# Kernel optimization log

Measured on AMD Instinct MI355X. Metric: run time of the kernel, lower is better.

## Reference

```python
import jax, jax.numpy as jnp
import numpy as np
from jax import lax

B, SEQ, CIN = 8, 4096, 7
DM, NL, PL = 512, 4, 16
NP = SEQ // PL            # 256 patches
NS, DC, EXP = 16, 4, 2
DI = EXP * DM             # 1024 inner dim
DTR = (DM + 15) // 16     # 32 dt_rank (mamba_ssm default ceil(d_model/16))
CD, PRED = 64, 96
EPS = 1e-5


def setup_inputs() -> dict:
    key = jax.random.key(0)
    ks = jax.random.split(key, 16)
    r = lambda k, s, sc=0.02: jax.random.normal(k, s, jnp.float32) * sc
    A_row = jnp.arange(1, NS + 1, dtype=jnp.float32)
    return {
        "x": jax.random.normal(ks[0], (B, SEQ, CIN), jnp.float32),
        "in_g": jnp.ones((CIN,), jnp.float32), "in_b": jnp.zeros((CIN,), jnp.float32),
        "pe_W": r(ks[1], (DM, CIN, PL), 0.1), "pe_b": jnp.zeros((DM,), jnp.float32),
        "ln_g": jnp.ones((NL, DM), jnp.float32), "ln_b": jnp.zeros((NL, DM), jnp.float32),
        "W_in": r(ks[2], (NL, 2 * DI, DM)),
        "conv_W": r(ks[3], (NL, DI, 1, DC), 0.2), "conv_b": jnp.zeros((NL, DI), jnp.float32),
        "W_x": r(ks[4], (NL, DTR + 2 * NS, DI)),
        "W_dt": r(ks[5], (NL, DI, DTR), 0.1),
        "b_dt": jnp.full((NL, DI), -4.6, jnp.float32),  # softplus^-1(~0.01)
        "A_log": jnp.log(jnp.tile(A_row, (NL, DI, 1))),
        "Dskip": jnp.ones((NL, DI), jnp.float32),
        "W_out": r(ks[6], (NL, DM, DI)),
        "fn_g": jnp.ones((DM,), jnp.float32), "fn_b": jnp.zeros((DM,), jnp.float32),
        "hW1": r(ks[7], (2 * CD, DM * NP)), "hb1": jnp.zeros((2 * CD,), jnp.float32),
        "hW2": r(ks[8], (PRED, 2 * CD)), "hb2": jnp.zeros((PRED,), jnp.float32),
    }


def layernorm(x, g, b):
    m = jnp.mean(x, axis=-1, keepdims=True)
    v = jnp.mean((x - m) ** 2, axis=-1, keepdims=True)
    return (x - m) * lax.rsqrt(v + EPS) * g + b


def silu(x):
    return x * jax.nn.sigmoid(x)


def selective_scan(dA, dBx, C):
    # dA, dBx: (B, L, DI, N);  C: (B, L, N)  ->  y: (B, L, DI)
    def step(h, t):
        dA_t, dbx_t, c_t = t
        h = dA_t * h + dbx_t                      # (B, DI, N)
        y = jnp.einsum('bdn,bn->bd', h, c_t)
        return h, y
    h0 = jnp.zeros((dA.shape[0], DI, NS), dA.dtype)
    _, ys = lax.scan(step, h0, (dA.transpose(1, 0, 2, 3), dBx.transpose(1, 0, 2, 3), C.transpose(1, 0, 2)))
    return ys.transpose(1, 0, 2)


def mamba_block(u, W_in, cW, cb, W_x, W_dt, b_dt, A_log, Dv, W_out):
    xz = jnp.einsum('bld,ed->ble', u, W_in)       # (B, L, 2*DI)
    xi, z = jnp.split(xz, 2, axis=-1)
    # causal depthwise conv over time
    xc = lax.conv_general_dilated(xi.transpose(0, 2, 1), cW, (1,), [(DC - 1, 0)],
                                  feature_group_count=DI,
                                  dimension_numbers=('NCH', 'OIH', 'NCH'))
    xc = silu(xc + cb[None, :, None]).transpose(0, 2, 1)  # (B, L, DI)
    dbl = jnp.einsum('bld,ed->ble', xc, W_x)      # (B, L, DTR + 2*NS)
    dt, Bm, Cm = dbl[..., :DTR], dbl[..., DTR:DTR + NS], dbl[..., DTR + NS:]
    delta = jax.nn.softplus(jnp.einsum('blr,dr->bld', dt, W_dt) + b_dt)  # (B, L, DI)
    A = -jnp.exp(A_log)                           # (DI, NS)
    dA = jnp.exp(delta[..., None] * A)            # (B, L, DI, NS)
    dBx = delta[..., None] * Bm[:, :, None, :] * xc[..., None]
    y = selective_scan(dA, dBx, Cm)
    y = (y + xc * Dv) * silu(z)
    return jnp.einsum('bld,od->blo', y, W_out)


def reference(x, in_g, in_b, pe_W, pe_b, ln_g, ln_b, W_in, conv_W, conv_b,
              W_x, W_dt, b_dt, A_log, Dskip, W_out, fn_g, fn_b, hW1, hb1, hW2, hb2):
    h = layernorm(x, in_g, in_b)
    # patch embed: stride==kernel Conv1d == per-patch matmul
    p = h.reshape(B, NP, PL, CIN)
    h = jnp.einsum('bnpc,dcp->bnd', p, pe_W) + pe_b   # (B, NP, DM)
    for i in range(NL):
        res = h
        h = layernorm(h, ln_g[i], ln_b[i])
        h = mamba_block(h, W_in[i], conv_W[i], conv_b[i], W_x[i], W_dt[i],
                        b_dt[i], A_log[i], Dskip[i], W_out[i])
        h = h + res                                   # dropout is identity at eval
    h = layernorm(h, fn_g, fn_b)
    h = h.reshape(B, -1)                              # (B, DM*NP)
    h = jax.nn.gelu(h @ hW1.T + hb1, approximate=False)
    return h @ hW2.T + hb2                            # (B, PRED)
```

## Files before the change

kernel.cpp:

```cpp
#include <hip/hip_runtime.h>
#include <hip/hip_bf16.h>
#include <math.h>

#define B_    8
#define SEQ_  4096
#define CIN_  7
#define DM_   512
#define NL_   4
#define PL_   16
#define NP_   256
#define NS_   16
#define DC_   4
#define DI_   1024
#define DTR_  32
#define CD_   64
#define PRED_ 96
#define TOK_  (B_*NP_)
#define EPS_  1e-5f
#define CL_   16
#define NCH_  (NP_/CL_)

typedef unsigned short u16;
typedef __attribute__((ext_vector_type(8))) short short8;
typedef __attribute__((ext_vector_type(4))) float floatx4;

__device__ __forceinline__ float silu_f(float x){ return x / (1.f + __expf(-x)); }
__device__ __forceinline__ float softplus_f(float x){ return x > 20.f ? x : log1pf(__expf(x)); }
__device__ __forceinline__ u16 f2bf(float f){
  union { __hip_bfloat16 h; u16 u; } cv; cv.h = __float2bfloat16(f); return cv.u;
}
#define GLDS16(g, l) __builtin_amdgcn_global_load_lds( \
    (const __attribute__((address_space(1))) void*)(g), \
    (__attribute__((address_space(3))) void*)(l), 16, 0, 0)

__global__ void ln7_kernel(const float* __restrict__ x, const float* __restrict__ g,
                           const float* __restrict__ b, u16* __restrict__ xpb){
  int i = blockIdx.x*256 + threadIdx.x;
  if (i >= B_*SEQ_) return;
  float v[CIN_]; float m = 0.f;
  #pragma unroll
  for (int c=0;c<CIN_;c++){ v[c]=x[i*CIN_+c]; m+=v[c]; }
  m *= (1.f/CIN_);
  float var = 0.f;
  #pragma unroll
  for (int c=0;c<CIN_;c++){ float d=v[c]-m; var+=d*d; }
  var *= (1.f/CIN_);
  float r = rsqrtf(var + EPS_);
  int bn = i >> 4, p = i & 15;
  u16* row = xpb + (size_t)bn*128;
  #pragma unroll
  for (int c=0;c<CIN_;c++) row[c*16+p] = f2bf((v[c]-m)*r*g[c]+b[c]);
  row[112+p] = 0;
}

__global__ __launch_bounds__(256) void ln512_kernel(const float* __restrict__ in,
    const float* __restrict__ g, const float* __restrict__ b,
    float* __restrict__ out, u16* __restrict__ outb){
  int tid = threadIdx.x;
  int wv = tid>>6, lane = tid&63;
  int t = blockIdx.x*4 + wv;
  const float4* row = (const float4*)(in + (size_t)t*DM_);
  float4 v0 = row[lane], v1 = row[64+lane];
  float s = v0.x+v0.y+v0.z+v0.w + v1.x+v1.y+v1.z+v1.w;
  #pragma unroll
  for (int o=1;o<64;o<<=1) s += __shfl_xor(s,o);
  float m = s*(1.f/DM_);
  float d0x=v0.x-m,d0y=v0.y-m,d0z=v0.z-m,d0w=v0.w-m;
  float d1x=v1.x-m,d1y=v1.y-m,d1z=v1.z-m,d1w=v1.w-m;
  float q = d0x*d0x+d0y*d0y+d0z*d0z+d0w*d0w + d1x*d1x+d1y*d1y+d1z*d1z+d1w*d1w;
  #pragma unroll
  for (int o=1;o<64;o<<=1) q += __shfl_xor(q,o);
  float r = rsqrtf(q*(1.f/DM_) + EPS_);
  float4 g0 = ((const float4*)g)[lane], g1 = ((const float4*)g)[64+lane];
  float4 b0 = ((const float4*)b)[lane], b1 = ((const float4*)b)[64+lane];
  float4 o0 = { d0x*r*g0.x+b0.x, d0y*r*g0.y+b0.y, d0z*r*g0.z+b0.z, d0w*r*g0.w+b0.w };
  float4 o1 = { d1x*r*g1.x+b1.x, d1y*r*g1.y+b1.y, d1z*r*g1.z+b1.z, d1w*r*g1.w+b1.w };
  ((float4*)(out + (size_t)t*DM_))[lane]    = o0;
  ((float4*)(out + (size_t)t*DM_))[64+lane] = o1;
  ushort4 p0 = { f2bf(o0.x), f2bf(o0.y), f2bf(o0.z), f2bf(o0.w) };
  ushort4 p1 = { f2bf(o1.x), f2bf(o1.y), f2bf(o1.z), f2bf(o1.w) };
  ((ushort4*)(outb + (size_t)t*DM_))[lane]    = p0;
  ((ushort4*)(outb + (size_t)t*DM_))[64+lane] = p1;
}

template<int BM, int BN, bool ACC, bool BIAS>
__global__ __launch_bounds__(256) void gemm_bf16(const u16* __restrict__ A,
    const u16* __restrict__ Bw, float* __restrict__ C, const float* __restrict__ bias,
    int K, int lda, int ldb, int ldc){
  constexpr int MI = BM/32, NI = BN/32;
  __shared__ __align__(16) u16 As[BM*64];
  __shared__ __align__(16) u16 Bs[BN*64];
  int tid = threadIdx.x;
  int wave = __builtin_amdgcn_readfirstlane(tid>>6);
  int lane = tid&63;
  int wm = wave>>1, wn = wave&1;
  int quad = lane>>4, l16 = lane&15;
  int bm = blockIdx.y*BM, bn = blockIdx.x*BN;
  int r8 = lane>>3, sseg = lane&7;
  int gseg = sseg ^ r8;
  floatx4 acc[MI][NI] = {};
  for (int k0 = 0; k0 < K; k0 += 64){
    #pragma unroll
    for (int r = 0; r < BM/32; r++){
      int rowb = (r*4 + wave)*8;
      const u16* gp = A + (size_t)(bm + rowb + r8)*lda + k0 + gseg*8;
      GLDS16(gp, &As[rowb*64]);
    }
    #pragma unroll
    for (int r = 0; r < BN/32; r++){
      int rowb = (r*4 + wave)*8;
      const u16* gp = Bw + (size_t)(bn + rowb + r8)*ldb + k0 + gseg*8;
      GLDS16(gp, &Bs[rowb*64]);
    }
    __syncthreads();
    #pragma unroll
    for (int kh = 0; kh < 2; kh++){
      short8 af[MI], bfr[NI];
      #pragma unroll
      for (int i = 0; i < MI; i++){
        int row = wm*(BM/2)+i*16+l16;
        af[i] = *(short8*)&As[row*64 + (((kh*4+quad)^(row&7))*8)];
      }
      #pragma unroll
      for (int j = 0; j < NI; j++){
        int row = wn*(BN/2)+j*16+l16;
        bfr[j] = *(short8*)&Bs[row*64 + (((kh*4+quad)^(row&7))*8)];
      }
      #pragma unroll
      for (int i = 0; i < MI; i++)
        #pragma unroll
        for (int j = 0; j < NI; j++)
          acc[i][j] = __builtin_amdgcn_mfma_f32_16x16x32_bf16(af[i], bfr[j], acc[i][j], 0, 0, 0);
    }
    __syncthreads();
  }
  #pragma unroll
  for (int i = 0; i < MI; i++){
    #pragma unroll
    for (int j = 0; j < NI; j++){
      #pragma unroll
      for (int r = 0; r < 4; r++){
        int m  = bm + wm*(BM/2) + i*16 + quad*4 + r;
        int nn = bn + wn*(BN/2) + j*16 + l16;
        float v = acc[i][j][r];
        if (ACC) C[(size_t)m*ldc+nn] += v;
        else     C[(size_t)m*ldc+nn]  = BIAS ? v + bias[nn] : v;
      }
    }
  }
}

__global__ __launch_bounds__(256) void mid_kernel(
    const float* __restrict__ xz, const float* __restrict__ cW, const float* __restrict__ cb,
    const float* __restrict__ wxT, const float* __restrict__ wdtT, const float* __restrict__ bdt,
    float* __restrict__ xc, float* __restrict__ dblo, float* __restrict__ delta){
  __shared__ float sxc[8*1024];
  __shared__ float swx[64*68];
  __shared__ float sdbl[8][64];
  int tid = threadIdx.x;
  int t0 = blockIdx.x*8;
  int l0 = t0 & (NP_-1);
  int c = tid*4;
  float w0[4], w1[4], w2[4], w3[4];
  *(float4*)w0 = *(const float4*)&cW[(c+0)*DC_];
  *(float4*)w1 = *(const float4*)&cW[(c+1)*DC_];
  *(float4*)w2 = *(const float4*)&cW[(c+2)*DC_];
  *(float4*)w3 = *(const float4*)&cW[(c+3)*DC_];
  float4 bias4 = *(const float4*)&cb[c];
  #pragma unroll
  for (int r = 0; r < 8; r++){
    float4 acc = bias4;
    int l = l0 + r;
    #pragma unroll
    for (int k = 0; k < DC_; k++){
      if (l - 3 + k >= 0){
        float4 xv = *(const float4*)&xz[(size_t)(t0 + r + k - 3)*(2*DI_) + c];
        acc.x += xv.x*w0[k]; acc.y += xv.y*w1[k]; acc.z += xv.z*w2[k]; acc.w += xv.w*w3[k];
      }
    }
    acc.x = silu_f(acc.x); acc.y = silu_f(acc.y); acc.z = silu_f(acc.z); acc.w = silu_f(acc.w);
    *(float4*)&sxc[r*1024 + c] = acc;
    *(float4*)&xc[(size_t)(t0+r)*DI_ + c] = acc;
  }
  int lane = tid & 63, wv = tid >> 6;
  int ta = wv*2, tb = ta + 1;
  float acc0 = 0.f, acc1 = 0.f;
  __syncthreads();
  for (int k0 = 0; k0 < DI_; k0 += 64){
    #pragma unroll
    for (int i = tid; i < 1024; i += 256){
      int k = i >> 4, e4 = (i & 15)*4;
      float4 v = *(const float4*)&wxT[(size_t)(k0 + k)*64 + e4];
      swx[(e4+0)*68 + k] = v.x;
      swx[(e4+1)*68 + k] = v.y;
      swx[(e4+2)*68 + k] = v.z;
      swx[(e4+3)*68 + k] = v.w;
    }
    __syncthreads();
    #pragma unroll
    for (int k4 = 0; k4 < 64; k4 += 4){
      float4 wq = *(float4*)&swx[lane*68 + k4];
      float4 xa = *(float4*)&sxc[ta*1024 + k0 + k4];
      float4 xb = *(float4*)&sxc[tb*1024 + k0 + k4];
      acc0 += xa.x*wq.x + xa.y*wq.y + xa.z*wq.z + xa.w*wq.w;
      acc1 += xb.x*wq.x + xb.y*wq.y + xb.z*wq.z + xb.w*wq.w;
    }
    __syncthreads();
  }
  sdbl[ta][lane] = acc0;
  sdbl[tb][lane] = acc1;
  dblo[(size_t)(t0+ta)*64 + lane] = acc0;
  dblo[(size_t)(t0+tb)*64 + lane] = acc1;
  __syncthreads();
  #pragma unroll
  for (int dc = 0; dc < 4; dc++){
    int d = dc*256 + tid;
    float wr[DTR_];
    #pragma unroll
    for (int r = 0; r < DTR_; r++) wr[r] = wdtT[(size_t)r*DI_ + d];
    float bb = bdt[d];
    #pragma unroll
    for (int t = 0; t < 8; t++){
      float acc = bb;
      #pragma unroll
      for (int r = 0; r < DTR_; r++) acc += sdbl[t][r]*wr[r];
      delta[(size_t)(t0+t)*DI_ + d] = softplus_f(acc);
    }
  }
}

__global__ __launch_bounds__(256) void scan_part_kernel(const float* __restrict__ delta,
    const float* __restrict__ xc, const float* __restrict__ dbl,
    const float* __restrict__ Alog, float* __restrict__ hend, float* __restrict__ aprod){
  __shared__ float sBC[CL_][32];
  int tid = threadIdx.x;
  int d = blockIdx.x*256 + tid;
  int bych = blockIdx.y;
  int b = bych >> 4, ch = bych & (NCH_-1);
  int base = b*NP_ + ch*CL_;
  for (int i = tid; i < CL_*32; i += 256){
    int t = i >> 5, c = i & 31;
    sBC[t][c] = dbl[(size_t)(base+t)*64 + 32 + c];
  }
  float A[NS_], h[NS_], pr[NS_];
  #pragma unroll
  for (int k = 0; k < NS_; k++){
    A[k] = -__expf(Alog[(size_t)d*NS_ + k]);
    h[k] = 0.f; pr[k] = 1.f;
  }
  __syncthreads();
  #pragma unroll
  for (int t = 0; t < CL_; t++){
    int row = base + t;
    float de = delta[(size_t)row*DI_ + d];
    float xv = xc[(size_t)row*DI_ + d];
    float cde = de*xv;
    #pragma unroll
    for (int k = 0; k < NS_; k++){
      float a = __expf(de*A[k]);
      h[k] = a*h[k] + cde*sBC[t][k];
      pr[k] *= a;
    }
  }
  size_t o = ((size_t)bych*DI_ + d)*NS_;
  #pragma unroll
  for (int k = 0; k < NS_; k++){ hend[o+k] = h[k]; aprod[o+k] = pr[k]; }
}

__global__ __launch_bounds__(256) void scan_fix_kernel(const float* __restrict__ aprod,
    float* __restrict__ hend){
  int id = blockIdx.x*256 + threadIdx.x;
  int nd = id & (DI_*NS_ - 1);
  int b  = id >> 14;
  float h = 0.f;
  #pragma unroll
  for (int ch = 0; ch < NCH_; ch++){
    size_t idx = (size_t)(b*NCH_ + ch)*(DI_*NS_) + nd;
    float ap = aprod[idx];
    float he = hend[idx];
    hend[idx] = h;
    h = ap*h + he;
  }
}

__global__ __launch_bounds__(256) void scan_final_kernel(const float* __restrict__ delta,
    const float* __restrict__ xc, const float* __restrict__ dbl,
    const float* __restrict__ xz, const float* __restrict__ Dv,
    const float* __restrict__ Alog, const float* __restrict__ hin,
    u16* __restrict__ yb){
  __shared__ float sBC[CL_][32];
  int tid = threadIdx.x;
  int d = blockIdx.x*256 + tid;
  int bych = blockIdx.y;
  int b = bych >> 4, ch = bych & (NCH_-1);
  int base = b*NP_ + ch*CL_;
  for (int i = tid; i < CL_*32; i += 256){
    int t = i >> 5, c = i & 31;
    sBC[t][c] = dbl[(size_t)(base+t)*64 + 32 + c];
  }
  float A[NS_], h[NS_];
  size_t o = ((size_t)bych*DI_ + d)*NS_;
  #pragma unroll
  for (int k = 0; k < NS_; k++){
    A[k] = -__expf(Alog[(size_t)d*NS_ + k]);
    h[k] = hin[o + k];
  }
  float Dvd = Dv[d];
  __syncthreads();
  #pragma unroll
  for (int t = 0; t < CL_; t++){
    int row = base + t;
    float de = delta[(size_t)row*DI_ + d];
    float xv = xc[(size_t)row*DI_ + d];
    float zz = xz[(size_t)row*(2*DI_) + DI_ + d];
    float cde = de*xv;
    float p = 0.f;
    #pragma unroll
    for (int k = 0; k < NS_; k++){
      float a = __expf(de*A[k]);
      h[k] = a*h[k] + cde*sBC[t][k];
      p += h[k]*sBC[t][16+k];
    }
    yb[(size_t)row*DI_ + d] = f2bf((p + xv*Dvd) * silu_f(zz));
  }
}

__global__ __launch_bounds__(256) void head1_kernel(const float* __restrict__ u,
    const float* __restrict__ hW1, float* __restrict__ partial){
  const int KTOT = DM_*NP_;
  int nb = blockIdx.x;
  int kc = blockIdx.y;
  int tid = threadIdx.x;
  int lane = tid & 63, wv = tid >> 6;
  int k = kc*1024 + tid*4;
  float4 uv[8];
  #pragma unroll
  for (int m = 0; m < 8; m++) uv[m] = *(const float4*)&u[(size_t)m*KTOT + k];
  float acc[8][8];
  #pragma unroll
  for (int n = 0; n < 8; n++){
    float4 wv4 = *(const float4*)&hW1[(size_t)(nb*8+n)*KTOT + k];
    #pragma unroll
    for (int m = 0; m < 8; m++)
      acc[n][m] = uv[m].x*wv4.x + uv[m].y*wv4.y + uv[m].z*wv4.z + uv[m].w*wv4.w;
  }
  __shared__ float red[4][64];
  #pragma unroll
  for (int n = 0; n < 8; n++){
    #pragma unroll
    for (int m = 0; m < 8; m++){
      float v = acc[n][m];
      v += __shfl_xor(v,1); v += __shfl_xor(v,2); v += __shfl_xor(v,4);
      v += __shfl_xor(v,8); v += __shfl_xor(v,16); v += __shfl_xor(v,32);
      if (lane == 0) red[wv][n*8+m] = v;
    }
  }
  __syncthreads();
  if (tid < 64){
    float s = red[0][tid] + red[1][tid] + red[2][tid] + red[3][tid];
    int n = tid >> 3, m = tid & 7;
    partial[((size_t)kc*128 + nb*8 + n)*8 + m] = s;
  }
}

__global__ void head_combine_kernel(const float* __restrict__ partial,
    const float* __restrict__ hb1, float* __restrict__ t1){
  int idx = blockIdx.x*256 + threadIdx.x;
  if (idx >= 128*8) return;
  int n = idx >> 3, m = idx & 7;
  float s = hb1[n];
  for (int kc = 0; kc < 128; kc++) s += partial[((size_t)kc*128 + n)*8 + m];
  float ge = 0.5f*s*(1.f + erff(s*0.70710678118f));
  t1[m*128 + n] = ge;
}

__global__ void head2_kernel(const float* __restrict__ t1, const float* __restrict__ hW2,
                             const float* __restrict__ hb2, float* __restrict__ out){
  int idx = blockIdx.x*128 + threadIdx.x;
  if (idx >= B_*PRED_) return;
  int m = idx / PRED_, q = idx % PRED_;
  float s = hb2[q];
  #pragma unroll 16
  for (int k = 0; k < 2*CD_; k++) s += t1[m*128 + k]*hW2[q*128 + k];
  out[idx] = s;
}

__global__ __launch_bounds__(256) void prep_kernel(const float* __restrict__ W_dt,
    const float* __restrict__ W_x, const float* __restrict__ W_in,
    const float* __restrict__ W_out, const float* __restrict__ peW,
    float* __restrict__ wdtT, float* __restrict__ wxT,
    u16* __restrict__ WinB, u16* __restrict__ WoutB, u16* __restrict__ peWb){
  int idx = blockIdx.x*256 + threadIdx.x;
  {
    float4 v = ((const float4*)W_in)[idx];
    ushort4 o = { f2bf(v.x), f2bf(v.y), f2bf(v.z), f2bf(v.w) };
    ((ushort4*)WinB)[idx] = o;
  }
  if (idx < 524288){
    float4 v = ((const float4*)W_out)[idx];
    ushort4 o = { f2bf(v.x), f2bf(v.y), f2bf(v.z), f2bf(v.w) };
    ((ushort4*)WoutB)[idx] = o;
  }
  if (idx < NL_*DTR_*DI_){
    int l = idx / (DTR_*DI_); int rem = idx % (DTR_*DI_);
    int r = rem / DI_; int d = rem % DI_;
    wdtT[idx] = W_dt[((size_t)l*DI_ + d)*DTR_ + r];
  }
  if (idx < NL_*DI_*64){
    int l = idx / (DI_*64); int rem = idx % (DI_*64);
    int kk = rem / 64; int e = rem % 64;
    wxT[idx] = W_x[((size_t)l*64 + e)*DI_ + kk];
  }
  if (idx < 512*128){
    int d = idx >> 7, kk = idx & 127;
    peWb[idx] = (kk < 112) ? f2bf(peW[d*112 + kk]) : (u16)0;
  }
}

extern "C" void kernel_launch(void* const* d_in, const int* in_sizes, int n_in,
                              void* d_out, int out_size, void* d_ws, size_t ws_size,
                              hipStream_t stream) {
  const float* x      = (const float*)d_in[0];
  const float* in_g   = (const float*)d_in[1];
  const float* in_b   = (const float*)d_in[2];
  const float* pe_W   = (const float*)d_in[3];
  const float* pe_b   = (const float*)d_in[4];
  const float* ln_g   = (const float*)d_in[5];
  const float* ln_b   = (const float*)d_in[6];
  const float* W_in   = (const float*)d_in[7];
  const float* conv_W = (const float*)d_in[8];
  const float* conv_b = (const float*)d_in[9];
  const float* W_x    = (const float*)d_in[10];
  const float* W_dt   = (const float*)d_in[11];
  const float* b_dt   = (const float*)d_in[12];
  const float* A_log  = (const float*)d_in[13];
  const float* Dskip  = (const float*)d_in[14];
  const float* W_out  = (const float*)d_in[15];
  const float* fn_g   = (const float*)d_in[16];
  const float* fn_b   = (const float*)d_in[17];
  const float* hW1    = (const float*)d_in[18];
  const float* hb1    = (const float*)d_in[19];
  const float* hW2    = (const float*)d_in[20];
  const float* hb2    = (const float*)d_in[21];

  float* ws    = (float*)d_ws;
  float* h     = ws;
  float* un    = h     + 1048576;
  float* xz    = un    + 1048576;
  float* xc    = xz    + 4194304;
  float* dblb  = xc    + 2097152;
  float* delta = dblb  + 131072;
  float* y     = delta + 2097152;
  float* wdtT  = y     + 2097152;
  float* wxT   = wdtT  + 131072;
  float* bf_rgn= wxT   + 262144;
  u16*   unb   = (u16*)bf_rgn;
  u16*   yb    = (u16*)(bf_rgn + 524288);
  u16*   WinB  = (u16*)(bf_rgn + 524288 + 1048576);
  u16*   WoutB = (u16*)(bf_rgn + 524288 + 1048576 + 2097152);
  u16*   peWb  = (u16*)(bf_rgn + 524288 + 1048576 + 2097152 + 1048576);
  float* aprod = bf_rgn + 524288 + 1048576 + 2097152 + 1048576 + 32768;
  float* hend  = y;
  u16*   xpb   = (u16*)y;
  float* partial = xz;
  float* t1      = xz + 262144;

  prep_kernel<<<4096, 256, 0, stream>>>(W_dt, W_x, W_in, W_out, pe_W,
                                        wdtT, wxT, WinB, WoutB, peWb);
  ln7_kernel<<<(B_*SEQ_+255)/256, 256, 0, stream>>>(x, in_g, in_b, xpb);
  gemm_bf16<64,128,false,true><<<dim3(DM_/128, TOK_/64), 256, 0, stream>>>(
      xpb, peWb, h, pe_b, 128, 128, 128, DM_);

  for (int l = 0; l < NL_; l++){
    ln512_kernel<<<TOK_/4, 256, 0, stream>>>(h, ln_g + l*DM_, ln_b + l*DM_, un, unb);
    gemm_bf16<64,128,false,false><<<dim3(2*DI_/128, TOK_/64), 256, 0, stream>>>(
        unb, WinB + (size_t)l*2*DI_*DM_, xz, nullptr, DM_, DM_, DM_, 2*DI_);
    mid_kernel<<<TOK_/8, 256, 0, stream>>>(
        xz, conv_W + (size_t)l*DI_*DC_, conv_b + (size_t)l*DI_,
        wxT + (size_t)l*DI_*64, wdtT + (size_t)l*DTR_*DI_, b_dt + (size_t)l*DI_,
        xc, dblb, delta);
    scan_part_kernel<<<dim3(DI_/256, B_*NCH_), 256, 0, stream>>>(
        delta, xc, dblb, A_log + (size_t)l*DI_*NS_, hend, aprod);
    scan_fix_kernel<<<(B_*DI_*NS_)/256, 256, 0, stream>>>(aprod, hend);
    scan_final_kernel<<<dim3(DI_/256, B_*NCH_), 256, 0, stream>>>(
        delta, xc, dblb, xz, Dskip + (size_t)l*DI_, A_log + (size_t)l*DI_*NS_, hend, yb);
    gemm_bf16<64,64,true,false><<<dim3(DM_/64, TOK_/64), 256, 0, stream>>>(
        yb, WoutB + (size_t)l*DM_*DI_, h, nullptr, DI_, DI_, DI_, DM_);
  }

  ln512_kernel<<<TOK_/4, 256, 0, stream>>>(h, fn_g, fn_b, un, unb);
  head1_kernel<<<dim3(16, 128), 256, 0, stream>>>(un, hW1, partial);
  head_combine_kernel<<<4, 256, 0, stream>>>(partial, hb1, t1);
  head2_kernel<<<6, 128, 0, stream>>>(t1, hW2, hb2, (float*)d_out);
}
```

Before: 671.7 us.

## Split mid kernel into conv, bf16 MFMA x_proj GEMM, and delta kernels

Replaces the fused conv+x_proj+dt_proj kernel with three kernels. A depthwise conv+SiLU kernel also writes a bf16 copy of xc, the x_proj projection runs through the existing bf16 MFMA GEMM with weights converted in prep, and a separate kernel computes delta. This moves the FP32 scalar dot products in shared memory onto matrix cores. In exchange it adds kernel launches, extra global traffic for xcb and dbl, bf16 rounding in the B/C/dt projections, and a x_proj GEMM grid of only 32 blocks.

```diff
diff --git a/kernel.cpp b/kernel.cpp
--- a/kernel.cpp
+++ b/kernel.cpp
@@ -150,82 +150,59 @@
   }
 }
 
-__global__ __launch_bounds__(256) void mid_kernel(
-    const float* __restrict__ xz, const float* __restrict__ cW, const float* __restrict__ cb,
-    const float* __restrict__ wxT, const float* __restrict__ wdtT, const float* __restrict__ bdt,
-    float* __restrict__ xc, float* __restrict__ dblo, float* __restrict__ delta){
-  __shared__ float sxc[8*1024];
-  __shared__ float swx[64*68];
-  __shared__ float sdbl[8][64];
-  int tid = threadIdx.x;
-  int t0 = blockIdx.x*8;
-  int l0 = t0 & (NP_-1);
-  int c = tid*4;
-  float w0[4], w1[4], w2[4], w3[4];
-  *(float4*)w0 = *(const float4*)&cW[(c+0)*DC_];
-  *(float4*)w1 = *(const float4*)&cW[(c+1)*DC_];
-  *(float4*)w2 = *(const float4*)&cW[(c+2)*DC_];
-  *(float4*)w3 = *(const float4*)&cW[(c+3)*DC_];
-  float4 bias4 = *(const float4*)&cb[c];
-  #pragma unroll
-  for (int r = 0; r < 8; r++){
-    float4 acc = bias4;
-    int l = l0 + r;
-    #pragma unroll
-    for (int k = 0; k < DC_; k++){
-      if (l - 3 + k >= 0){
-        float4 xv = *(const float4*)&xz[(size_t)(t0 + r + k - 3)*(2*DI_) + c];
-        acc.x += xv.x*w0[k]; acc.y += xv.y*w1[k]; acc.z += xv.z*w2[k]; acc.w += xv.w*w3[k];
-      }
-    }
-    acc.x = silu_f(acc.x); acc.y = silu_f(acc.y); acc.z = silu_f(acc.z); acc.w = silu_f(acc.w);
-    *(float4*)&sxc[r*1024 + c] = acc;
-    *(float4*)&xc[(size_t)(t0+r)*DI_ + c] = acc;
-  }
-  int lane = tid & 63, wv = tid >> 6;
-  int ta = wv*2, tb = ta + 1;
-  float acc0 = 0.f, acc1 = 0.f;
+__global__ void conv_silu_kernel(const float* __restrict__ xz, const float* __restrict__ cW,
+                                 const float* __restrict__ cb, float* __restrict__ xc,
+                                 u16* __restrict__ xcb){
+  int idx = blockIdx.x*256 + threadIdx.x;
+  if (idx >= TOK_*DI_/4) return;
+  int c4 = idx & (DI_/4 - 1); int t = idx >> 8;
+  int l = t & (NP_-1);
+  int c = c4*4;
+  float4 acc = *(const float4*)&cb[c];
+  float wa[4], wb[4], wc[4], wd[4];
+  *(float4*)wa = *(const float4*)&cW[(c+0)*DC_];
+  *(float4*)wb = *(const float4*)&cW[(c+1)*DC_];
+  *(float4*)wc = *(const float4*)&cW[(c+2)*DC_];
+  *(float4*)wd = *(const float4*)&cW[(c+3)*DC_];
+  const float* base = xz + (size_t)t*(2*DI_) + c;
+  #pragma unroll
+  for (int k = 0; k < DC_; k++){
+    if (l - 3 + k >= 0){
+      float4 xv = *(const float4*)(base + (k-3)*(2*DI_));
+      acc.x += xv.x*wa[k];
+      acc.y += xv.y*wb[k];
+      acc.z += xv.z*wc[k];
+      acc.w += xv.w*wd[k];
+    }
+  }
+  acc.x = silu_f(acc.x); acc.y = silu_f(acc.y);
+  acc.z = silu_f(acc.z); acc.w = silu_f(acc.w);
+  *(float4*)&xc[(size_t)t*DI_ + c] = acc;
+  ushort4 pb = { f2bf(acc.x), f2bf(acc.y), f2bf(acc.z), f2bf(acc.w) };
+  *(ushort4*)&xcb[(size_t)t*DI_ + c] = pb;
+}
+
+__global__ __launch_bounds__(256) void delta_kernel(const float* __restrict__ dbl,
+    const float* __restrict__ wdtT, const float* __restrict__ bdt, float* __restrict__ delta){
+  __shared__ float sdt[16][DTR_];
+  int tid = threadIdx.x;
+  int t0 = blockIdx.y*16;
+  int d = blockIdx.x*256 + tid;
+  for (int i = tid; i < 16*DTR_; i += 256){
+    int t = i >> 5, r = i & 31;
+    sdt[t][r] = dbl[(size_t)(t0 + t)*64 + r];
+  }
+  float wv[DTR_];
+  #pragma unroll
+  for (int r = 0; r < DTR_; r++) wv[r] = wdtT[(size_t)r*DI_ + d];
+  float bb = bdt[d];
   __syncthreads();
-  for (int k0 = 0; k0 < DI_; k0 += 64){
-    #pragma unroll
-    for (int i = tid; i < 1024; i += 256){
-      int k = i >> 4, e4 = (i & 15)*4;
-      float4 v = *(const float4*)&wxT[(size_t)(k0 + k)*64 + e4];
-      swx[(e4+0)*68 + k] = v.x;
-      swx[(e4+1)*68 + k] = v.y;
-      swx[(e4+2)*68 + k] = v.z;
-      swx[(e4+3)*68 + k] = v.w;
-    }
-    __syncthreads();
-    #pragma unroll
-    for (int k4 = 0; k4 < 64; k4 += 4){
-      float4 wq = *(float4*)&swx[lane*68 + k4];
-      float4 xa = *(float4*)&sxc[ta*1024 + k0 + k4];
-      float4 xb = *(float4*)&sxc[tb*1024 + k0 + k4];
-      acc0 += xa.x*wq.x + xa.y*wq.y + xa.z*wq.z + xa.w*wq.w;
-      acc1 += xb.x*wq.x + xb.y*wq.y + xb.z*wq.z + xb.w*wq.w;
-    }
-    __syncthreads();
-  }
-  sdbl[ta][lane] = acc0;
-  sdbl[tb][lane] = acc1;
-  dblo[(size_t)(t0+ta)*64 + lane] = acc0;
-  dblo[(size_t)(t0+tb)*64 + lane] = acc1;
-  __syncthreads();
-  #pragma unroll
-  for (int dc = 0; dc < 4; dc++){
-    int d = dc*256 + tid;
-    float wr[DTR_];
-    #pragma unroll
-    for (int r = 0; r < DTR_; r++) wr[r] = wdtT[(size_t)r*DI_ + d];
-    float bb = bdt[d];
-    #pragma unroll
-    for (int t = 0; t < 8; t++){
-      float acc = bb;
-      #pragma unroll
-      for (int r = 0; r < DTR_; r++) acc += sdbl[t][r]*wr[r];
-      delta[(size_t)(t0+t)*DI_ + d] = softplus_f(acc);
-    }
+  #pragma unroll 4
+  for (int t = 0; t < 16; t++){
+    float acc = bb;
+    #pragma unroll
+    for (int r = 0; r < DTR_; r++) acc += sdt[t][r]*wv[r];
+    delta[(size_t)(t0 + t)*DI_ + d] = softplus_f(acc);
   }
 }
 
@@ -388,7 +365,7 @@
 __global__ __launch_bounds__(256) void prep_kernel(const float* __restrict__ W_dt,
     const float* __restrict__ W_x, const float* __restrict__ W_in,
     const float* __restrict__ W_out, const float* __restrict__ peW,
-    float* __restrict__ wdtT, float* __restrict__ wxT,
+    float* __restrict__ wdtT, u16* __restrict__ wxB,
     u16* __restrict__ WinB, u16* __restrict__ WoutB, u16* __restrict__ peWb){
   int idx = blockIdx.x*256 + threadIdx.x;
   {
@@ -401,15 +378,15 @@
     ushort4 o = { f2bf(v.x), f2bf(v.y), f2bf(v.z), f2bf(v.w) };
     ((ushort4*)WoutB)[idx] = o;
   }
+  if (idx < NL_*64*DI_/4){
+    float4 v = ((const float4*)W_x)[idx];
+    ushort4 o = { f2bf(v.x), f2bf(v.y), f2bf(v.z), f2bf(v.w) };
+    ((ushort4*)wxB)[idx] = o;
+  }
   if (idx < NL_*DTR_*DI_){
     int l = idx / (DTR_*DI_); int rem = idx % (DTR_*DI_);
     int r = rem / DI_; int d = rem % DI_;
     wdtT[idx] = W_dt[((size_t)l*DI_ + d)*DTR_ + r];
-  }
-  if (idx < NL_*DI_*64){
-    int l = idx / (DI_*64); int rem = idx % (DI_*64);
-    int kk = rem / 64; int e = rem % 64;
-    wxT[idx] = W_x[((size_t)l*64 + e)*DI_ + kk];
   }
   if (idx < 512*128){
     int d = idx >> 7, kk = idx & 127;
@@ -452,8 +429,8 @@
   float* delta = dblb  + 131072;
   float* y     = delta + 2097152;
   float* wdtT  = y     + 2097152;
-  float* wxT   = wdtT  + 131072;
-  float* bf_rgn= wxT   + 262144;
+  u16*   wxB   = (u16*)(wdtT + 131072);
+  float* bf_rgn= wdtT + 131072 + 131072;
   u16*   unb   = (u16*)bf_rgn;
   u16*   yb    = (u16*)(bf_rgn + 524288);
   u16*   WinB  = (u16*)(bf_rgn + 524288 + 1048576);
@@ -461,12 +438,13 @@
   u16*   peWb  = (u16*)(bf_rgn + 524288 + 1048576 + 2097152 + 1048576);
   float* aprod = bf_rgn + 524288 + 1048576 + 2097152 + 1048576 + 32768;
   float* hend  = y;
+  u16*   xcb   = (u16*)y;
   u16*   xpb   = (u16*)y;
   float* partial = xz;
   float* t1      = xz + 262144;
 
   prep_kernel<<<4096, 256, 0, stream>>>(W_dt, W_x, W_in, W_out, pe_W,
-                                        wdtT, wxT, WinB, WoutB, peWb);
+                                        wdtT, wxB, WinB, WoutB, peWb);
   ln7_kernel<<<(B_*SEQ_+255)/256, 256, 0, stream>>>(x, in_g, in_b, xpb);
   gemm_bf16<64,128,false,true><<<dim3(DM_/128, TOK_/64), 256, 0, stream>>>(
       xpb, peWb, h, pe_b, 128, 128, 128, DM_);
@@ -475,10 +453,12 @@
     ln512_kernel<<<TOK_/4, 256, 0, stream>>>(h, ln_g + l*DM_, ln_b + l*DM_, un, unb);
     gemm_bf16<64,128,false,false><<<dim3(2*DI_/128, TOK_/64), 256, 0, stream>>>(
         unb, WinB + (size_t)l*2*DI_*DM_, xz, nullptr, DM_, DM_, DM_, 2*DI_);
-    mid_kernel<<<TOK_/8, 256, 0, stream>>>(
-        xz, conv_W + (size_t)l*DI_*DC_, conv_b + (size_t)l*DI_,
-        wxT + (size_t)l*DI_*64, wdtT + (size_t)l*DTR_*DI_, b_dt + (size_t)l*DI_,
-        xc, dblb, delta);
+    conv_silu_kernel<<<(TOK_*DI_/4)/256, 256, 0, stream>>>(
+        xz, conv_W + (size_t)l*DI_*DC_, conv_b + (size_t)l*DI_, xc, xcb);
+    gemm_bf16<64,64,false,false><<<dim3(1, TOK_/64), 256, 0, stream>>>(
+        xcb, wxB + (size_t)l*64*DI_, dblb, nullptr, DI_, DI_, DI_, 64);
+    delta_kernel<<<dim3(DI_/256, TOK_/16), 256, 0, stream>>>(
+        dblb, wdtT + (size_t)l*DTR_*DI_, b_dt + (size_t)l*DI_, delta);
     scan_part_kernel<<<dim3(DI_/256, B_*NCH_), 256, 0, stream>>>(
         delta, xc, dblb, A_log + (size_t)l*DI_*NS_, hend, aprod);
     scan_fix_kernel<<<(B_*DI_*NS_)/256, 256, 0, stream>>>(aprod, hend);
```

Result: faster. 603.4 us (-10.2%).
